# Performance work log

Measured on AMD Instinct MI355X. Metric: run time of the kernel, lower is better.

## Reference

```python
import jax, jax.numpy as jnp
import numpy as np

B, V, T, N = 2, 50000, 3, 32
F, FE, U, E = 128, 128, 128, 300000
NEG_FILL = -200.0
LEAKY_ALPHA = 0.3  # keras.layers.LeakyReLU default


def setup_inputs() -> dict:
    key = jax.random.key(0)
    ks = jax.random.split(key, 9)
    adjacency = jax.random.randint(ks[0], (B, V, T, N), 0, V).astype(jnp.int32)
    features = jax.random.normal(ks[1], (B, V, F), jnp.float32)
    bi = jax.random.randint(ks[2], (T, E), 0, B)
    vi = jax.random.randint(ks[3], (T, E), 0, V)
    si = jax.random.randint(ks[4], (T, E), 0, N)
    edge_idxs = jnp.stack([bi, vi, si], axis=-1).astype(jnp.int32)  # (batch, dst_vertex, slot)
    edge_feats = jax.random.normal(ks[5], (T, E, FE), jnp.float32)
    W_dense = jax.random.normal(ks[6], (T, FE, U), jnp.float32) * (1.0 / np.sqrt(FE))
    b_dense = jnp.zeros((T, U), jnp.float32)
    W_att = jax.random.normal(ks[7], (F + U, 1), jnp.float32) * 0.05
    b_att = jnp.zeros((1,), jnp.float32)
    return {"adjacency": adjacency, "features": features, "edge_idxs": edge_idxs,
            "edge_feats": edge_feats, "W_dense": W_dense, "b_dense": b_dense,
            "W_att": W_att, "b_att": b_att}


def reference(adjacency, features, edge_idxs, edge_feats, W_dense, b_dense, W_att, b_att):
    Bv, Vv, Tv, Nv = adjacency.shape
    Tt, Ee, _ = edge_idxs.shape
    Uu = W_dense.shape[-1]
    b = edge_idxs[..., 0]  # [T,E]
    v = edge_idxs[..., 1]
    s = edge_idxs[..., 2]
    t = jnp.broadcast_to(jnp.arange(Tv, dtype=edge_idxs.dtype)[:, None], (Tv, Ee))
    # per-edge-type linear transform of edge features
    xform = jnp.einsum('tef,tfu->teu', edge_feats, W_dense) + b_dense[:, None, :]  # [T,E,U]
    # destination-vertex node features gathered per edge
    src = features[b, v]  # [T,E,F]
    att_in = jnp.concatenate([src, xform], axis=-1)  # [T,E,F+U]
    logits = jax.nn.leaky_relu(att_in @ W_att + b_att, negative_slope=LEAKY_ALPHA)[..., 0]  # [T,E]
    # scatter logits into dense neighbour grid, softmax over all (edge_type, slot) pairs
    atts = jnp.full((Bv, Vv, Tv, Nv), NEG_FILL, dtype=logits.dtype)
    atts = atts.at[b, v, t, s].set(logits)
    atts = jax.nn.softmax(atts.reshape(Bv, Vv, Tv * Nv), axis=-1).reshape(Bv, Vv, Tv, Nv)
    edge_atts = atts[b, v, t, s][..., None]  # [T,E,1]
    weighted = (xform * edge_atts).reshape(Tv * Ee, Uu)
    # scatter-add over (batch, vertex) == scatter_nd to [B,V,N,U] then sum over slot axis
    out = jnp.zeros((Bv, Vv, Uu), weighted.dtype).at[b.reshape(-1), v.reshape(-1)].add(weighted)
    # use_sum=True, group_edges=False: multiply by total degree over all edge types/slots
    degree = jnp.sum((adjacency >= 0).astype(jnp.int32), axis=(-1, -2)).astype(out.dtype)[..., None]
    return out * degree
```

## Files before the change

kernel.cpp:

```cpp
#include <hip/hip_runtime.h>
#include <cstdint>

#define ALPHA 0.3f
#define NEG_FILL -200.0f

typedef unsigned short ushort_t;
typedef __attribute__((ext_vector_type(8))) short bf16x8;
typedef __attribute__((ext_vector_type(4))) float f32x4;

constexpr int Bc = 2, Vc = 50000, Tc = 3, Nc = 32;
constexpr int Fc = 128, FEc = 128, Uc = 128, Ec = 300000;
constexpr int TNc = Tc * Nc;
constexpr int BVc = Bc * Vc;
constexpr int TEc = Tc * Ec;
constexpr int CAP = 64;

__device__ __forceinline__ ushort_t f2bf(float f) {
    unsigned u = __float_as_uint(f);
    return (ushort_t)((u + 0x7fffu + ((u >> 16) & 1u)) >> 16);
}
__device__ __forceinline__ float bf2f(ushort_t b) {
    return __uint_as_float(((unsigned)b) << 16);
}

__global__ __launch_bounds__(256) void k_wprep(
    const float* __restrict__ Wd, ushort_t* __restrict__ Wt)
{
    const int g = blockIdx.x * 256 + threadIdx.x;
    if (g >= Tc * 2048) return;
    const int t = g >> 11, rem = g & 2047;
    const int kt = rem >> 10, gi = rem & 1023;
    const int u = gi >> 3, pos = gi & 7;
    const int kq = pos ^ (u & 7);
    const float* Ws = Wd + (size_t)t * FEc * Uc;
    bf16x8 val;
#pragma unroll
    for (int j = 0; j < 8; ++j)
        val[j] = (short)f2bf(Ws[(size_t)(kt * 64 + kq * 8 + j) * Uc + u]);
    *(bf16x8*)&Wt[(size_t)g * 8] = val;
}

__global__ __launch_bounds__(256) void k_gemm(
    const float* __restrict__ ef, const ushort_t* __restrict__ Wt,
    const float* __restrict__ bd, const float* __restrict__ Wa,
    ushort_t* __restrict__ xform, float* __restrict__ dotx)
{
    __shared__ ushort_t sA[128 * 64];
    __shared__ ushort_t sW[128 * 64];
    const int t   = blockIdx.y;
    const int e0  = blockIdx.x * 128;
    const int tid = threadIdx.x;
    const int wave = tid >> 6, lane = tid & 63;
    const int ln = lane & 15, quad = lane >> 4;
    const int m0 = (wave >> 1) * 64, n0 = (wave & 1) * 64;

    f32x4 acc[4][4];
#pragma unroll
    for (int i = 0; i < 4; ++i)
#pragma unroll
        for (int j = 0; j < 4; ++j)
#pragma unroll
            for (int r = 0; r < 4; ++r) acc[i][j][r] = 0.f;

    const float*    Ab = ef + ((size_t)t * Ec + e0) * FEc;
    const ushort_t* Wb = Wt + (size_t)t * 16384;

    for (int kt = 0; kt < 2; ++kt) {
        __syncthreads();
#pragma unroll
        for (int it = 0; it < 4; ++it) {
            const int g = tid + it * 256;
            const int row = g >> 3, pos = g & 7;
            const int kq = pos ^ (row & 7);
            bf16x8 val;
            if (e0 + row < Ec) {
                const float* s = Ab + (size_t)row * FEc + kt * 64 + kq * 8;
                float4 f0 = *(const float4*)s;
                float4 f1 = *(const float4*)(s + 4);
                val[0] = (short)f2bf(f0.x); val[1] = (short)f2bf(f0.y);
                val[2] = (short)f2bf(f0.z); val[3] = (short)f2bf(f0.w);
                val[4] = (short)f2bf(f1.x); val[5] = (short)f2bf(f1.y);
                val[6] = (short)f2bf(f1.z); val[7] = (short)f2bf(f1.w);
            } else {
#pragma unroll
                for (int q = 0; q < 8; ++q) val[q] = 0;
            }
            *(bf16x8*)&sA[(size_t)g * 8] = val;
            *(bf16x8*)&sW[(size_t)g * 8] = *(const bf16x8*)&Wb[(size_t)(kt * 1024 + g) * 8];
        }
        __syncthreads();
#pragma unroll
        for (int kk = 0; kk < 2; ++kk) {
            bf16x8 af[4], bfr[4];
            const int p = (kk * 4 + quad) ^ (ln & 7);
#pragma unroll
            for (int i = 0; i < 4; ++i) {
                const int row = m0 + i * 16 + ln;
                af[i] = *(const bf16x8*)&sA[(size_t)(row * 8 + p) * 8];
            }
#pragma unroll
            for (int j = 0; j < 4; ++j) {
                const int row = n0 + j * 16 + ln;
                bfr[j] = *(const bf16x8*)&sW[(size_t)(row * 8 + p) * 8];
            }
#pragma unroll
            for (int i = 0; i < 4; ++i)
#pragma unroll
                for (int j = 0; j < 4; ++j)
                    acc[i][j] = __builtin_amdgcn_mfma_f32_16x16x32_bf16(
                        af[i], bfr[j], acc[i][j], 0, 0, 0);
        }
    }

    float bdv[4], wav[4];
#pragma unroll
    for (int j = 0; j < 4; ++j) {
        const int u = n0 + j * 16 + ln;
        bdv[j] = bd[t * Uc + u];
        wav[j] = Wa[Fc + u];
    }
#pragma unroll
    for (int i = 0; i < 4; ++i) {
#pragma unroll
        for (int r = 0; r < 4; ++r) {
            const int e = e0 + m0 + i * 16 + quad * 4 + r;
            if (e < Ec) {
                const size_t base = ((size_t)t * Ec + e) * Uc;
                float p = 0.f;
#pragma unroll
                for (int j = 0; j < 4; ++j) {
                    const float v = acc[i][j][r] + bdv[j];
                    xform[base + n0 + j * 16 + ln] = f2bf(v);
                    p += v * wav[j];
                }
                p += __shfl_xor(p, 1); p += __shfl_xor(p, 2);
                p += __shfl_xor(p, 4); p += __shfl_xor(p, 8);
                if (ln == 0) atomicAdd(&dotx[t * Ec + e], p);
            }
        }
    }
}

__global__ __launch_bounds__(256) void k_fdot(
    const float* __restrict__ feat, const float* __restrict__ Wa,
    float* __restrict__ fdot)
{
    const int wv = blockIdx.x * 4 + (threadIdx.x >> 6);
    const int lane = threadIdx.x & 63;
    if (wv >= BVc) return;
    const float* fr = feat + (size_t)wv * Fc;
    float p = fr[lane] * Wa[lane] + fr[lane + 64] * Wa[lane + 64];
#pragma unroll
    for (int x = 1; x < 64; x <<= 1) p += __shfl_xor(p, x);
    if (lane == 0) fdot[wv] = p;
}

__global__ __launch_bounds__(256) void k_prep(
    const int* __restrict__ eidx, const float* __restrict__ fdot,
    const float* __restrict__ dotx, const float* __restrict__ ba,
    float* __restrict__ logits, int* __restrict__ keyg,
    int* __restrict__ cnt, int* __restrict__ elist)
{
    const int i = blockIdx.x * 256 + threadIdx.x;
    if (i >= TEc) return;
    const int b = eidx[i * 3 + 0];
    const int v = eidx[i * 3 + 1];
    const int s = eidx[i * 3 + 2];
    const int t = i / Ec;
    const int vtx = b * Vc + v;
    const float z = fdot[vtx] + dotx[i] + ba[0];
    logits[i] = (z >= 0.f) ? z : ALPHA * z;
    atomicMax(&keyg[(size_t)vtx * TNc + t * Nc + s], i);
    const int pos = atomicAdd(&cnt[vtx], 1);
    if (pos < CAP) elist[(size_t)vtx * CAP + pos] = i | (s << 20);
}

__global__ __launch_bounds__(128) void k_vertex(
    const int* __restrict__ adj, const int* __restrict__ keyg,
    const float* __restrict__ logits, const int* __restrict__ cnt,
    const int* __restrict__ elist, const ushort_t* __restrict__ xform,
    float* __restrict__ out)
{
    const int vtx = blockIdx.x;
    const int tid = threadIdx.x;
    const int wave = tid >> 6, lane = tid & 63;
    __shared__ float att[TNc];
    __shared__ float redf[2];
    __shared__ float reds[2];
    __shared__ int   redi[2];

    float l = -1e30f;
    int dg = 0;
    if (tid < TNc) {
        const int k = keyg[(size_t)vtx * TNc + tid];
        l = (k >= 0) ? logits[k] : NEG_FILL;
        dg = (adj[(size_t)vtx * TNc + tid] >= 0) ? 1 : 0;
    }
    float m = l; int d = dg;
#pragma unroll
    for (int x = 1; x < 64; x <<= 1) {
        m = fmaxf(m, __shfl_xor(m, x));
        d += __shfl_xor(d, x);
    }
    if (lane == 0) { redf[wave] = m; redi[wave] = d; }
    __syncthreads();
    m = fmaxf(redf[0], redf[1]);
    const float degree = (float)(redi[0] + redi[1]);
    float e = (tid < TNc) ? expf(l - m) : 0.f;
    float sum = e;
#pragma unroll
    for (int x = 1; x < 64; x <<= 1) sum += __shfl_xor(sum, x);
    if (lane == 0) reds[wave] = sum;
    __syncthreads();
    const float invden = 1.0f / (reds[0] + reds[1]);
    if (tid < TNc) att[tid] = e * invden;
    __syncthreads();

    const int ne = min(cnt[vtx], CAP);
    float acc = 0.f;
    for (int it = 0; it < ne; ++it) {
        const int packed = elist[(size_t)vtx * CAP + it];
        const int eid = packed & 0xFFFFF;
        const int s   = packed >> 20;
        const float w = att[(eid / Ec) * Nc + s];
        acc += w * bf2f(xform[(size_t)eid * Uc + tid]);
    }
    out[(size_t)vtx * Uc + tid] = acc * degree;
}

extern "C" void kernel_launch(void* const* d_in, const int* in_sizes, int n_in,
                              void* d_out, int out_size, void* d_ws, size_t ws_size,
                              hipStream_t stream)
{
    const int*   adj  = (const int*)  d_in[0];
    const float* feat = (const float*)d_in[1];
    const int*   eidx = (const int*)  d_in[2];
    const float* ef   = (const float*)d_in[3];
    const float* Wd   = (const float*)d_in[4];
    const float* bd   = (const float*)d_in[5];
    const float* Wa   = (const float*)d_in[6];
    const float* ba   = (const float*)d_in[7];
    float* out = (float*)d_out;

    char* ws = (char*)d_ws;
    ushort_t* xform  = (ushort_t*)ws; ws += (size_t)TEc * Uc * 2;
    float*    dotx   = (float*)ws;    ws += (size_t)TEc * 4;
    float*    logits = (float*)ws;    ws += (size_t)TEc * 4;
    int*      keyg   = (int*)ws;      ws += (size_t)BVc * TNc * 4;
    float*    fdot   = (float*)ws;    ws += (size_t)BVc * 4;
    int*      cnt    = (int*)ws;      ws += (size_t)BVc * 4;
    int*      elist  = (int*)ws;      ws += (size_t)BVc * CAP * 4;
    ushort_t* Wt     = (ushort_t*)ws; ws += (size_t)Tc * 16384 * 2;

    hipMemsetAsync(keyg, 0xFF, (size_t)BVc * TNc * 4, stream);
    hipMemsetAsync(cnt, 0, (size_t)BVc * 4, stream);
    hipMemsetAsync(dotx, 0, (size_t)TEc * 4, stream);

    k_wprep<<<(Tc * 2048 + 255) / 256, 256, 0, stream>>>(Wd, Wt);
    dim3 g1((Ec + 127) / 128, Tc);
    k_gemm<<<g1, 256, 0, stream>>>(ef, Wt, bd, Wa, xform, dotx);
    k_fdot<<<(BVc + 3) / 4, 256, 0, stream>>>(feat, Wa, fdot);
    k_prep<<<(TEc + 255) / 256, 256, 0, stream>>>(eidx, fdot, dotx, ba, logits, keyg, cnt, elist);
    k_vertex<<<BVc, 128, 0, stream>>>(adj, keyg, logits, cnt, elist, xform, out);
}
```

Before: 1.001 ms.

## Aggregate raw edge features per vertex before the dense transform

```diff
diff --git a/kernel.cpp b/kernel.cpp
--- a/kernel.cpp
+++ b/kernel.cpp
@@ -13,14 +13,12 @@
 constexpr int TNc = Tc * Nc;
 constexpr int BVc = Bc * Vc;
 constexpr int TEc = Tc * Ec;
+constexpr int KTOT = Tc * FEc;
 constexpr int CAP = 64;
 
 __device__ __forceinline__ ushort_t f2bf(float f) {
     unsigned u = __float_as_uint(f);
     return (ushort_t)((u + 0x7fffu + ((u >> 16) & 1u)) >> 16);
-}
-__device__ __forceinline__ float bf2f(ushort_t b) {
-    return __uint_as_float(((unsigned)b) << 16);
 }
 
 __global__ __launch_bounds__(256) void k_wprep(
@@ -40,14 +38,147 @@
     *(bf16x8*)&Wt[(size_t)g * 8] = val;
 }
 
-__global__ __launch_bounds__(256) void k_gemm(
-    const float* __restrict__ ef, const ushort_t* __restrict__ Wt,
-    const float* __restrict__ bd, const float* __restrict__ Wa,
-    ushort_t* __restrict__ xform, float* __restrict__ dotx)
+__global__ __launch_bounds__(128) void k_wv(
+    const float* __restrict__ Wd, const float* __restrict__ bd,
+    const float* __restrict__ Wa, const float* __restrict__ ba,
+    float* __restrict__ wv, float* __restrict__ ct)
+{
+    const int t = blockIdx.x, f = threadIdx.x;
+    const float* W = Wd + (size_t)t * FEc * Uc + (size_t)f * Uc;
+    float acc = 0.f;
+    for (int u = 0; u < Uc; ++u) acc += W[u] * Wa[Fc + u];
+    wv[t * FEc + f] = acc;
+    if (f == 0) {
+        float c = ba[0];
+        for (int u = 0; u < Uc; ++u) c += bd[t * Uc + u] * Wa[Fc + u];
+        ct[t] = c;
+    }
+}
+
+__global__ __launch_bounds__(256) void k_fdot(
+    const float* __restrict__ feat, const float* __restrict__ Wa,
+    float* __restrict__ fdot)
+{
+    const int wv = blockIdx.x * 4 + (threadIdx.x >> 6);
+    const int lane = threadIdx.x & 63;
+    if (wv >= BVc) return;
+    const float* fr = feat + (size_t)wv * Fc;
+    float p = fr[lane] * Wa[lane] + fr[lane + 64] * Wa[lane + 64];
+#pragma unroll
+    for (int x = 1; x < 64; x <<= 1) p += __shfl_xor(p, x);
+    if (lane == 0) fdot[wv] = p;
+}
+
+__global__ __launch_bounds__(256) void k_edge(
+    const int* __restrict__ eidx, const float* __restrict__ ef,
+    const float* __restrict__ wv, const float* __restrict__ ct,
+    const float* __restrict__ fdot, float* __restrict__ logits,
+    int* __restrict__ cnt, int* __restrict__ elist)
+{
+    const int w = blockIdx.x * 4 + (threadIdx.x >> 6);
+    const int lane = threadIdx.x & 63;
+    if (w >= TEc) return;
+    const int t = w / Ec;
+    const float2 efv = *(const float2*)&ef[(size_t)w * FEc + lane * 2];
+    const float2 wvv = *(const float2*)&wv[t * FEc + lane * 2];
+    float p = efv.x * wvv.x + efv.y * wvv.y;
+#pragma unroll
+    for (int x = 1; x < 64; x <<= 1) p += __shfl_xor(p, x);
+    const int ev = (lane < 3) ? eidx[(size_t)w * 3 + lane] : 0;
+    const int b = __shfl(ev, 0);
+    const int v = __shfl(ev, 1);
+    const int s = __shfl(ev, 2);
+    if (lane == 0) {
+        const int vtx = b * Vc + v;
+        float z = p + ct[t] + fdot[vtx];
+        logits[w] = (z >= 0.f) ? z : ALPHA * z;
+        const int pos = atomicAdd(&cnt[vtx], 1);
+        if (pos < CAP) elist[(size_t)vtx * CAP + pos] = w | (s << 20) | (t << 25);
+    }
+}
+
+__global__ __launch_bounds__(128) void k_vertex(
+    const int* __restrict__ adj, const float* __restrict__ logits,
+    const int* __restrict__ cnt, const int* __restrict__ elist,
+    const float* __restrict__ ef, float* __restrict__ agg,
+    float4* __restrict__ s4)
+{
+    const int vtx = blockIdx.x;
+    const int tid = threadIdx.x;
+    const int wave = tid >> 6, lane = tid & 63;
+    __shared__ int   skey[TNc];
+    __shared__ int   epack[CAP];
+    __shared__ float att[TNc];
+    __shared__ float redf[2];
+    __shared__ float reds[2];
+    __shared__ int   redi[2];
+    __shared__ float sS[3];
+
+    const int ne = min(cnt[vtx], CAP);
+    if (tid < TNc) skey[tid] = -1;
+    if (tid < 3)   sS[tid] = 0.f;
+    __syncthreads();
+    if (tid < ne) {
+        const int p = elist[(size_t)vtx * CAP + tid];
+        epack[tid] = p;
+        atomicMax(&skey[((p >> 25) & 3) * Nc + ((p >> 20) & 31)], p & 0xFFFFF);
+    }
+    __syncthreads();
+
+    float l = -1e30f; int dg = 0;
+    if (tid < TNc) {
+        const int k = skey[tid];
+        l = (k >= 0) ? logits[k] : NEG_FILL;
+        dg = (adj[(size_t)vtx * TNc + tid] >= 0) ? 1 : 0;
+    }
+    float m = l; int d = dg;
+#pragma unroll
+    for (int x = 1; x < 64; x <<= 1) {
+        m = fmaxf(m, __shfl_xor(m, x));
+        d += __shfl_xor(d, x);
+    }
+    if (lane == 0) { redf[wave] = m; redi[wave] = d; }
+    __syncthreads();
+    m = fmaxf(redf[0], redf[1]);
+    const float degree = (float)(redi[0] + redi[1]);
+    float e = (tid < TNc) ? expf(l - m) : 0.f;
+    float sum = e;
+#pragma unroll
+    for (int x = 1; x < 64; x <<= 1) sum += __shfl_xor(sum, x);
+    if (lane == 0) reds[wave] = sum;
+    __syncthreads();
+    const float invden = 1.0f / (reds[0] + reds[1]);
+    if (tid < TNc) att[tid] = e * invden;
+    __syncthreads();
+
+    if (tid < ne) {
+        const int p = epack[tid];
+        atomicAdd(&sS[(p >> 25) & 3], att[((p >> 25) & 3) * Nc + ((p >> 20) & 31)]);
+    }
+    float a0 = 0.f, a1 = 0.f, a2 = 0.f;
+    for (int it = 0; it < ne; ++it) {
+        const int p = epack[it];
+        const int eid = p & 0xFFFFF;
+        const int t = (p >> 25) & 3;
+        const float w = att[t * Nc + ((p >> 20) & 31)];
+        const float x = ef[(size_t)eid * FEc + tid];
+        if (t == 0) a0 += w * x; else if (t == 1) a1 += w * x; else a2 += w * x;
+    }
+    __syncthreads();
+    const size_t base = (size_t)vtx * KTOT;
+    agg[base + tid]           = a0;
+    agg[base + FEc + tid]     = a1;
+    agg[base + 2 * FEc + tid] = a2;
+    if (tid == 0) s4[vtx] = make_float4(sS[0], sS[1], sS[2], degree);
+}
+
+__global__ __launch_bounds__(256) void k_out(
+    const float* __restrict__ agg, const ushort_t* __restrict__ Wt,
+    const float* __restrict__ bd, const float4* __restrict__ s4,
+    float* __restrict__ out)
 {
     __shared__ ushort_t sA[128 * 64];
     __shared__ ushort_t sW[128 * 64];
-    const int t   = blockIdx.y;
     const int e0  = blockIdx.x * 128;
     const int tid = threadIdx.x;
     const int wave = tid >> 6, lane = tid & 63;
@@ -62,10 +193,8 @@
 #pragma unroll
             for (int r = 0; r < 4; ++r) acc[i][j][r] = 0.f;
 
-    const float*    Ab = ef + ((size_t)t * Ec + e0) * FEc;
-    const ushort_t* Wb = Wt + (size_t)t * 16384;
-
-    for (int kt = 0; kt < 2; ++kt) {
+    for (int c = 0; c < 6; ++c) {
+        const int t = c >> 1, kt = c & 1;
         __syncthreads();
 #pragma unroll
         for (int it = 0; it < 4; ++it) {
@@ -73,8 +202,8 @@
             const int row = g >> 3, pos = g & 7;
             const int kq = pos ^ (row & 7);
             bf16x8 val;
-            if (e0 + row < Ec) {
-                const float* s = Ab + (size_t)row * FEc + kt * 64 + kq * 8;
+            if (e0 + row < BVc) {
+                const float* s = agg + (size_t)(e0 + row) * KTOT + t * FEc + kt * 64 + kq * 8;
                 float4 f0 = *(const float4*)s;
                 float4 f1 = *(const float4*)(s + 4);
                 val[0] = (short)f2bf(f0.x); val[1] = (short)f2bf(f0.y);
@@ -86,7 +215,7 @@
                 for (int q = 0; q < 8; ++q) val[q] = 0;
             }
             *(bf16x8*)&sA[(size_t)g * 8] = val;
-            *(bf16x8*)&sW[(size_t)g * 8] = *(const bf16x8*)&Wb[(size_t)(kt * 1024 + g) * 8];
+            *(bf16x8*)&sW[(size_t)g * 8] = *(const bf16x8*)&Wt[(size_t)(c * 1024 + g) * 8];
         }
         __syncthreads();
 #pragma unroll
@@ -112,120 +241,30 @@
         }
     }
 
-    float bdv[4], wav[4];
+    float bdv0[4], bdv1[4], bdv2[4];
 #pragma unroll
     for (int j = 0; j < 4; ++j) {
         const int u = n0 + j * 16 + ln;
-        bdv[j] = bd[t * Uc + u];
-        wav[j] = Wa[Fc + u];
+        bdv0[j] = bd[u];
+        bdv1[j] = bd[Uc + u];
+        bdv2[j] = bd[2 * Uc + u];
     }
 #pragma unroll
     for (int i = 0; i < 4; ++i) {
 #pragma unroll
         for (int r = 0; r < 4; ++r) {
             const int e = e0 + m0 + i * 16 + quad * 4 + r;
-            if (e < Ec) {
-                const size_t base = ((size_t)t * Ec + e) * Uc;
-                float p = 0.f;
+            if (e < BVc) {
+                const float4 sv = s4[e];
 #pragma unroll
                 for (int j = 0; j < 4; ++j) {
-                    const float v = acc[i][j][r] + bdv[j];
-                    xform[base + n0 + j * 16 + ln] = f2bf(v);
-                    p += v * wav[j];
+                    const float val = (acc[i][j][r] + sv.x * bdv0[j] + sv.y * bdv1[j]
+                                       + sv.z * bdv2[j]) * sv.w;
+                    out[(size_t)e * Uc + n0 + j * 16 + ln] = val;
                 }
-                p += __shfl_xor(p, 1); p += __shfl_xor(p, 2);
-                p += __shfl_xor(p, 4); p += __shfl_xor(p, 8);
-                if (ln == 0) atomicAdd(&dotx[t * Ec + e], p);
             }
         }
     }
-}
-
-__global__ __launch_bounds__(256) void k_fdot(
-    const float* __restrict__ feat, const float* __restrict__ Wa,
-    float* __restrict__ fdot)
-{
-    const int wv = blockIdx.x * 4 + (threadIdx.x >> 6);
-    const int lane = threadIdx.x & 63;
-    if (wv >= BVc) return;
-    const float* fr = feat + (size_t)wv * Fc;
-    float p = fr[lane] * Wa[lane] + fr[lane + 64] * Wa[lane + 64];
-#pragma unroll
-    for (int x = 1; x < 64; x <<= 1) p += __shfl_xor(p, x);
-    if (lane == 0) fdot[wv] = p;
-}
-
-__global__ __launch_bounds__(256) void k_prep(
-    const int* __restrict__ eidx, const float* __restrict__ fdot,
-    const float* __restrict__ dotx, const float* __restrict__ ba,
-    float* __restrict__ logits, int* __restrict__ keyg,
-    int* __restrict__ cnt, int* __restrict__ elist)
-{
-    const int i = blockIdx.x * 256 + threadIdx.x;
-    if (i >= TEc) return;
-    const int b = eidx[i * 3 + 0];
-    const int v = eidx[i * 3 + 1];
-    const int s = eidx[i * 3 + 2];
-    const int t = i / Ec;
-    const int vtx = b * Vc + v;
-    const float z = fdot[vtx] + dotx[i] + ba[0];
-    logits[i] = (z >= 0.f) ? z : ALPHA * z;
-    atomicMax(&keyg[(size_t)vtx * TNc + t * Nc + s], i);
-    const int pos = atomicAdd(&cnt[vtx], 1);
-    if (pos < CAP) elist[(size_t)vtx * CAP + pos] = i | (s << 20);
-}
-
-__global__ __launch_bounds__(128) void k_vertex(
-    const int* __restrict__ adj, const int* __restrict__ keyg,
-    const float* __restrict__ logits, const int* __restrict__ cnt,
-    const int* __restrict__ elist, const ushort_t* __restrict__ xform,
-    float* __restrict__ out)
-{
-    const int vtx = blockIdx.x;
-    const int tid = threadIdx.x;
-    const int wave = tid >> 6, lane = tid & 63;
-    __shared__ float att[TNc];
-    __shared__ float redf[2];
-    __shared__ float reds[2];
-    __shared__ int   redi[2];
-
-    float l = -1e30f;
-    int dg = 0;
-    if (tid < TNc) {
-        const int k = keyg[(size_t)vtx * TNc + tid];
-        l = (k >= 0) ? logits[k] : NEG_FILL;
-        dg = (adj[(size_t)vtx * TNc + tid] >= 0) ? 1 : 0;
-    }
-    float m = l; int d = dg;
-#pragma unroll
-    for (int x = 1; x < 64; x <<= 1) {
-        m = fmaxf(m, __shfl_xor(m, x));
-        d += __shfl_xor(d, x);
-    }
-    if (lane == 0) { redf[wave] = m; redi[wave] = d; }
-    __syncthreads();
-    m = fmaxf(redf[0], redf[1]);
-    const float degree = (float)(redi[0] + redi[1]);
-    float e = (tid < TNc) ? expf(l - m) : 0.f;
-    float sum = e;
-#pragma unroll
-    for (int x = 1; x < 64; x <<= 1) sum += __shfl_xor(sum, x);
-    if (lane == 0) reds[wave] = sum;
-    __syncthreads();
-    const float invden = 1.0f / (reds[0] + reds[1]);
-    if (tid < TNc) att[tid] = e * invden;
-    __syncthreads();
-
-    const int ne = min(cnt[vtx], CAP);
-    float acc = 0.f;
-    for (int it = 0; it < ne; ++it) {
-        const int packed = elist[(size_t)vtx * CAP + it];
-        const int eid = packed & 0xFFFFF;
-        const int s   = packed >> 20;
-        const float w = att[(eid / Ec) * Nc + s];
-        acc += w * bf2f(xform[(size_t)eid * Uc + tid]);
-    }
-    out[(size_t)vtx * Uc + tid] = acc * degree;
 }
 
 extern "C" void kernel_launch(void* const* d_in, const int* in_sizes, int n_in,
@@ -243,23 +282,22 @@
     float* out = (float*)d_out;
 
     char* ws = (char*)d_ws;
-    ushort_t* xform  = (ushort_t*)ws; ws += (size_t)TEc * Uc * 2;
-    float*    dotx   = (float*)ws;    ws += (size_t)TEc * 4;
     float*    logits = (float*)ws;    ws += (size_t)TEc * 4;
-    int*      keyg   = (int*)ws;      ws += (size_t)BVc * TNc * 4;
-    float*    fdot   = (float*)ws;    ws += (size_t)BVc * 4;
+    float*    agg    = (float*)ws;    ws += (size_t)BVc * KTOT * 4;
+    float4*   s4     = (float4*)ws;   ws += (size_t)BVc * 16;
     int*      cnt    = (int*)ws;      ws += (size_t)BVc * 4;
     int*      elist  = (int*)ws;      ws += (size_t)BVc * CAP * 4;
+    float*    fdot   = (float*)ws;    ws += (size_t)BVc * 4;
+    float*    wv     = (float*)ws;    ws += (size_t)Tc * FEc * 4;
+    float*    ctb    = (float*)ws;    ws += 16;
     ushort_t* Wt     = (ushort_t*)ws; ws += (size_t)Tc * 16384 * 2;
 
-    hipMemsetAsync(keyg, 0xFF, (size_t)BVc * TNc * 4, stream);
     hipMemsetAsync(cnt, 0, (size_t)BVc * 4, stream);
-    hipMemsetAsync(dotx, 0, (size_t)TEc * 4, stream);
 
     k_wprep<<<(Tc * 2048 + 255) / 256, 256, 0, stream>>>(Wd, Wt);
-    dim3 g1((Ec + 127) / 128, Tc);
-    k_gemm<<<g1, 256, 0, stream>>>(ef, Wt, bd, Wa, xform, dotx);
-    k_fdot<<<(BVc + 3) / 4, 256, 0, stream>>>(feat, Wa, fdot);
-    k_prep<<<(TEc + 255) / 256, 256, 0, stream>>>(eidx, fdot, dotx, ba, logits, keyg, cnt, elist);
-    k_vertex<<<BVc, 128, 0, stream>>>(adj, keyg, logits, cnt, elist, xform, out);
-}
+    k_wv<<<Tc, 128, 0, stream>>>(Wd, bd, Wa, ba, wv, ctb);
+    k_fdot<<<BVc / 4, 256, 0, stream>>>(feat, Wa, fdot);
+    k_edge<<<TEc / 4, 256, 0, stream>>>(eidx, ef, wv, ctb, fdot, logits, cnt, elist);
+    k_vertex<<<BVc, 128, 0, stream>>>(adj, logits, cnt, elist, ef, agg, s4);
+    k_out<<<(BVc + 127) / 128, 256, 0, stream>>>(agg, Wt, bd, s4, out);
+}
```

New measurement: 1.151 ms. +15.0%, slower.
